# Performance work log

Hardware: AMD Instinct MI355X
Metric: run time of the kernel (lower is better)

Reference implementation:

```python
import jax, jax.numpy as jnp
import numpy as np

VOCAB, H, E, B, S = 50257, 1024, 1024, 64, 2048


def setup_inputs() -> dict:
    key = jax.random.key(0)
    ks = jax.random.split(key, 12)
    s = 0.02
    return {
        "input_seq": jax.random.randint(ks[0], (B,), 0, VOCAB),
        "last_hidden": jax.random.normal(ks[1], (1, B, H), jnp.float32),
        "last_cell": jax.random.normal(ks[2], (1, B, H), jnp.float32),
        "encoder_outputs": jax.random.normal(ks[3], (S, B, H), jnp.float32),
        "emb_W": jax.random.normal(ks[4], (VOCAB, E), jnp.float32) * s,
        "W_ih": jax.random.normal(ks[5], (4 * H, E), jnp.float32) * s,
        "W_hh": jax.random.normal(ks[6], (4 * H, H), jnp.float32) * s,
        "b_ih": jnp.zeros((4 * H,), jnp.float32),
        "b_hh": jnp.zeros((4 * H,), jnp.float32),
        "concat_W": jax.random.normal(ks[7], (H, 2 * H), jnp.float32) * s,
        "concat_b": jnp.zeros((H,), jnp.float32),
        "out_W": jax.random.normal(ks[8], (VOCAB, H), jnp.float32) * s,
        "out_b": jnp.zeros((VOCAB,), jnp.float32),
    }


def reference(input_seq, last_hidden, last_cell, encoder_outputs,
              emb_W, W_ih, W_hh, b_ih, b_hh,
              concat_W, concat_b, out_W, out_b):
    # Embedding lookup (dropout is identity in eval mode)
    x = emb_W[input_seq]                      # [B, E]
    h0 = last_hidden[0]                       # [B, H]
    c0 = last_cell[0]                         # [B, H]
    # Single LSTM step (PyTorch gate order: i, f, g, o)
    gates = x @ W_ih.T + b_ih + h0 @ W_hh.T + b_hh   # [B, 4H]
    i, f, g, o = jnp.split(gates, 4, axis=-1)
    c = jax.nn.sigmoid(f) * c0 + jax.nn.sigmoid(i) * jnp.tanh(g)
    h = jax.nn.sigmoid(o) * jnp.tanh(c)       # [B, H] == rnn_output
    # 'dot' attention: energies[b, s] = h[b] . enc[s, b]  (vectorized)
    energies = jnp.einsum('bh,sbh->bs', h, encoder_outputs)   # [B, S]
    attn = jax.nn.softmax(energies, axis=1)                   # [B, S]
    context = jnp.einsum('bs,sbh->bh', attn, encoder_outputs) # [B, H]
    concat_out = jnp.tanh(jnp.concatenate([h, context], axis=1) @ concat_W.T + concat_b)
    output = concat_out @ out_W.T + out_b                     # [B, VOCAB]
    return output, h[None], c[None], attn[:, None, :]
```

## Files before the change

### kernel.cpp

```cpp
#include <hip/hip_runtime.h>
#include <hip/hip_bf16.h>
#include <math.h>

#define BB 64
#define HH 1024
#define SS 2048
#define VV 50257

typedef float f32x4 __attribute__((ext_vector_type(4)));
typedef short bf16x8 __attribute__((ext_vector_type(8)));

__device__ __forceinline__ float sigf(float x){ return 1.0f/(1.0f+__expf(-x)); }
__device__ __forceinline__ short f2bf(float f){
  __hip_bfloat16 h = __float2bfloat16(f);
  return __builtin_bit_cast(short, h);
}

__global__ __launch_bounds__(256)
void k_gates(const int* __restrict__ seq, const float* __restrict__ embW,
             const float* __restrict__ h0,
             const float* __restrict__ W_ih, const float* __restrict__ W_hh,
             float* __restrict__ dst)
{
  __shared__ float As[64][33];
  __shared__ float Ws[128][33];
  const int tid = threadIdx.x;
  const int nb = blockIdx.x, sk = blockIdx.y, SK = gridDim.y;
  const int tps = 64 / SK;
  const int t0 = sk * tps;
  const int bg = tid & 15, ng = tid >> 4;

  float acc[4][8];
  #pragma unroll
  for (int i = 0; i < 4; ++i)
    #pragma unroll
    for (int j = 0; j < 8; ++j) acc[i][j] = 0.f;

  const int ar = tid >> 2, ac = (tid & 3) * 8;
  const int wr = tid >> 1, wc = (tid & 1) * 16;
  const int wn = nb * 128 + wr;
  const int erow = seq[ar];

  for (int t = t0; t < t0 + tps; ++t) {
    const int kt = t << 5;
    const float* abase; const float* wbase;
    if (kt < 1024) {
      abase = embW + (size_t)erow*1024 + kt;
      wbase = W_ih + (size_t)wn*1024 + kt;
    } else {
      abase = h0 + (size_t)ar*1024 + (kt - 1024);
      wbase = W_hh + (size_t)wn*1024 + (kt - 1024);
    }
    {
      const float* s = abase + ac;
      float4 v0 = *(const float4*)s;
      float4 v1 = *(const float4*)(s + 4);
      As[ar][ac+0]=v0.x; As[ar][ac+1]=v0.y; As[ar][ac+2]=v0.z; As[ar][ac+3]=v0.w;
      As[ar][ac+4]=v1.x; As[ar][ac+5]=v1.y; As[ar][ac+6]=v1.z; As[ar][ac+7]=v1.w;
    }
    {
      const float* s = wbase + wc;
      float4 v0 = *(const float4*)s;
      float4 v1 = *(const float4*)(s + 4);
      float4 v2 = *(const float4*)(s + 8);
      float4 v3 = *(const float4*)(s + 12);
      Ws[wr][wc+0]=v0.x;  Ws[wr][wc+1]=v0.y;  Ws[wr][wc+2]=v0.z;  Ws[wr][wc+3]=v0.w;
      Ws[wr][wc+4]=v1.x;  Ws[wr][wc+5]=v1.y;  Ws[wr][wc+6]=v1.z;  Ws[wr][wc+7]=v1.w;
      Ws[wr][wc+8]=v2.x;  Ws[wr][wc+9]=v2.y;  Ws[wr][wc+10]=v2.z; Ws[wr][wc+11]=v2.w;
      Ws[wr][wc+12]=v3.x; Ws[wr][wc+13]=v3.y; Ws[wr][wc+14]=v3.z; Ws[wr][wc+15]=v3.w;
    }
    __syncthreads();
    #pragma unroll 8
    for (int k = 0; k < 32; ++k) {
      const float a0 = As[bg*4+0][k], a1 = As[bg*4+1][k];
      const float a2 = As[bg*4+2][k], a3 = As[bg*4+3][k];
      #pragma unroll
      for (int j = 0; j < 8; ++j) {
        const float w = Ws[ng*8+j][k];
        acc[0][j] += a0*w; acc[1][j] += a1*w; acc[2][j] += a2*w; acc[3][j] += a3*w;
      }
    }
    __syncthreads();
  }

  #pragma unroll
  for (int j = 0; j < 8; ++j) {
    const int n = nb*128 + ng*8 + j;
    #pragma unroll
    for (int i = 0; i < 4; ++i)
      dst[((size_t)sk*64 + (bg*4+i))*4096 + n] = acc[i][j];
  }
}

__global__ void k_rlstm(const float* __restrict__ part, const float* __restrict__ b_ih,
                        const float* __restrict__ b_hh, const float* __restrict__ c0,
                        float* __restrict__ h_out, float* __restrict__ c_out,
                        short* __restrict__ concA, int SK){
  int idx = blockIdx.x*256 + threadIdx.x;
  int b = idx >> 10, k = idx & 1023;
  float gi = b_ih[k]      + b_hh[k];
  float gf = b_ih[1024+k] + b_hh[1024+k];
  float gg = b_ih[2048+k] + b_hh[2048+k];
  float go = b_ih[3072+k] + b_hh[3072+k];
  const float* p = part + (size_t)b*4096 + k;
  for (int s = 0; s < SK; ++s) {
    const float* ps = p + (size_t)s*64*4096;
    gi += ps[0]; gf += ps[1024]; gg += ps[2048]; go += ps[3072];
  }
  float c = sigf(gf)*c0[idx] + sigf(gi)*tanhf(gg);
  float h = sigf(go)*tanhf(c);
  c_out[idx] = c;
  h_out[idx] = h;
  concA[(size_t)b*2048 + k] = f2bf(h);
}

__global__ __launch_bounds__(256)
void k_mfma(const short* __restrict__ A, int lda,
            const float* __restrict__ W1, int ldw,
            float* __restrict__ dst, int N, int Ktot)
{
  const int tid  = threadIdx.x;
  const int wave = tid >> 6, lane = tid & 63;
  const int nb = blockIdx.x, sk = blockIdx.y, SK = gridDim.y;
  const int ksteps = Ktot >> 5;
  const int kps = ksteps / SK;
  const int k0 = sk * kps;
  const int n0 = nb*128 + wave*32;
  const int r = lane & 15, g = lane >> 4;

  f32x4 acc[4][2] = {};

  for (int ks = k0; ks < k0 + kps; ++ks) {
    const int kk = (ks << 5) + g*8;
    bf16x8 af[4];
    #pragma unroll
    for (int mf = 0; mf < 4; ++mf)
      af[mf] = *(const bf16x8*)(A + (size_t)(mf*16 + r)*lda + kk);
    #pragma unroll
    for (int nf = 0; nf < 2; ++nf) {
      const int n = n0 + nf*16 + r;
      const float* wp = W1 + (size_t)n*ldw + kk;
      float4 w0 = *(const float4*)wp;
      float4 w1 = *(const float4*)(wp + 4);
      bf16x8 bfr;
      bfr[0]=f2bf(w0.x); bfr[1]=f2bf(w0.y); bfr[2]=f2bf(w0.z); bfr[3]=f2bf(w0.w);
      bfr[4]=f2bf(w1.x); bfr[5]=f2bf(w1.y); bfr[6]=f2bf(w1.z); bfr[7]=f2bf(w1.w);
      #pragma unroll
      for (int mf = 0; mf < 4; ++mf)
        acc[mf][nf] = __builtin_amdgcn_mfma_f32_16x16x32_bf16(af[mf], bfr, acc[mf][nf], 0, 0, 0);
    }
  }

  #pragma unroll
  for (int nf = 0; nf < 2; ++nf) {
    const int n = n0 + nf*16 + r;
    #pragma unroll
    for (int mf = 0; mf < 4; ++mf)
      #pragma unroll
      for (int j = 0; j < 4; ++j)
        dst[((size_t)sk*64 + (mf*16 + g*4 + j))*N + n] = acc[mf][nf][j];
  }
}

__global__ void k_reduce(const float* __restrict__ part, const float* __restrict__ bias,
                         short* __restrict__ dstb, int N, int SK){
  size_t idx = (size_t)blockIdx.x*256 + threadIdx.x;
  if (idx >= (size_t)64*N) return;
  int b = (int)(idx / N), n = (int)(idx % N);
  float v = bias[n];
  for (int s = 0; s < SK; ++s) v += part[((size_t)s*64 + b)*N + n];
  dstb[(size_t)b*N + n] = f2bf(tanhf(v));
}

__global__ __launch_bounds__(256)
void k_logits(const short* __restrict__ A, const float* __restrict__ W,
              const float* __restrict__ bias, float* __restrict__ out)
{
  const int tid = threadIdx.x;
  const int wave = tid >> 6, lane = tid & 63;
  const int r = lane & 15, g = lane >> 4;
  const int n0 = blockIdx.x*128 + wave*32;
  const int nA = n0 + r, nB = n0 + 16 + r;
  const float* wA = W + (size_t)(nA < VV ? nA : 0)*1024;
  const float* wB = W + (size_t)(nB < VV ? nB : 0)*1024;
  const short* A0 = A + (size_t)r*1024 + g*8;

  f32x4 acc[4][2] = {};

  bf16x8 a0,a1,a2,a3; float4 u0,u1,v0,v1;
  {
    const int kk = g*8;
    a0 = *(const bf16x8*)(A0);
    a1 = *(const bf16x8*)(A0 + 16*1024);
    a2 = *(const bf16x8*)(A0 + 32*1024);
    a3 = *(const bf16x8*)(A0 + 48*1024);
    u0 = *(const float4*)(wA + kk); u1 = *(const float4*)(wA + kk + 4);
    v0 = *(const float4*)(wB + kk); v1 = *(const float4*)(wB + kk + 4);
  }

  #pragma unroll
  for (int ks = 0; ks < 32; ++ks) {
    bf16x8 ca0=a0, ca1=a1, ca2=a2, ca3=a3;
    float4 cu0=u0, cu1=u1, cv0=v0, cv1=v1;
    if (ks < 31) {
      const int kk = (ks+1)*32 + g*8;
      a0 = *(const bf16x8*)(A0 + (ks+1)*32);
      a1 = *(const bf16x8*)(A0 + 16*1024 + (ks+1)*32);
      a2 = *(const bf16x8*)(A0 + 32*1024 + (ks+1)*32);
      a3 = *(const bf16x8*)(A0 + 48*1024 + (ks+1)*32);
      u0 = *(const float4*)(wA + kk); u1 = *(const float4*)(wA + kk + 4);
      v0 = *(const float4*)(wB + kk); v1 = *(const float4*)(wB + kk + 4);
    }
    bf16x8 bA, bB;
    bA[0]=f2bf(cu0.x); bA[1]=f2bf(cu0.y); bA[2]=f2bf(cu0.z); bA[3]=f2bf(cu0.w);
    bA[4]=f2bf(cu1.x); bA[5]=f2bf(cu1.y); bA[6]=f2bf(cu1.z); bA[7]=f2bf(cu1.w);
    bB[0]=f2bf(cv0.x); bB[1]=f2bf(cv0.y); bB[2]=f2bf(cv0.z); bB[3]=f2bf(cv0.w);
    bB[4]=f2bf(cv1.x); bB[5]=f2bf(cv1.y); bB[6]=f2bf(cv1.z); bB[7]=f2bf(cv1.w);
    acc[0][0] = __builtin_amdgcn_mfma_f32_16x16x32_bf16(ca0, bA, acc[0][0], 0,0,0);
    acc[1][0] = __builtin_amdgcn_mfma_f32_16x16x32_bf16(ca1, bA, acc[1][0], 0,0,0);
    acc[2][0] = __builtin_amdgcn_mfma_f32_16x16x32_bf16(ca2, bA, acc[2][0], 0,0,0);
    acc[3][0] = __builtin_amdgcn_mfma_f32_16x16x32_bf16(ca3, bA, acc[3][0], 0,0,0);
    acc[0][1] = __builtin_amdgcn_mfma_f32_16x16x32_bf16(ca0, bB, acc[0][1], 0,0,0);
    acc[1][1] = __builtin_amdgcn_mfma_f32_16x16x32_bf16(ca1, bB, acc[1][1], 0,0,0);
    acc[2][1] = __builtin_amdgcn_mfma_f32_16x16x32_bf16(ca2, bB, acc[2][1], 0,0,0);
    acc[3][1] = __builtin_amdgcn_mfma_f32_16x16x32_bf16(ca3, bB, acc[3][1], 0,0,0);
  }

  #pragma unroll
  for (int nf = 0; nf < 2; ++nf) {
    const int n = n0 + nf*16 + r;
    if (n < VV) {
      const float bv = bias[n];
      #pragma unroll
      for (int mf = 0; mf < 4; ++mf)
        #pragma unroll
        for (int j = 0; j < 4; ++j)
          out[(size_t)(mf*16 + g*4 + j)*VV + n] = acc[mf][nf][j] + bv;
    }
  }
}

__global__ __launch_bounds__(256)
void k_attn_part(const float* __restrict__ h, const float* __restrict__ enc,
                 float* __restrict__ energ, float* __restrict__ mpart,
                 float* __restrict__ lpart, float* __restrict__ ctxpart, int C){
  const int b  = blockIdx.x & 63;
  const int ch = blockIdx.x >> 6;
  const int wave = threadIdx.x >> 6;
  const int lane = threadIdx.x & 63;
  const int rows = SS / C;
  const int rpw  = rows >> 2;
  const int sw = ch*rows + wave*rpw;

  float4 hv0, hv1, hv2, hv3;
  {
    const float* hb = h + (size_t)b*HH + lane*16;
    hv0 = *(const float4*)(hb);   hv1 = *(const float4*)(hb+4);
    hv2 = *(const float4*)(hb+8); hv3 = *(const float4*)(hb+12);
  }
  float m = -INFINITY, l = 0.f;
  float cacc[16];
  #pragma unroll
  for (int j = 0; j < 16; ++j) cacc[j] = 0.f;

  for (int i = 0; i < rpw; i += 2) {
    const float* ep = enc + ((size_t)(sw+i)*BB + b)*HH + lane*16;
    const float* fp = ep + (size_t)BB*HH;
    const float4 e0 = *(const float4*)(ep);
    const float4 e1 = *(const float4*)(ep+4);
    const float4 e2 = *(const float4*)(ep+8);
    const float4 e3 = *(const float4*)(ep+12);
    const float4 f0 = *(const float4*)(fp);
    const float4 f1 = *(const float4*)(fp+4);
    const float4 f2 = *(const float4*)(fp+8);
    const float4 f3 = *(const float4*)(fp+12);
    float p = hv0.x*e0.x + hv0.y*e0.y + hv0.z*e0.z + hv0.w*e0.w
            + hv1.x*e1.x + hv1.y*e1.y + hv1.z*e1.z + hv1.w*e1.w
            + hv2.x*e2.x + hv2.y*e2.y + hv2.z*e2.z + hv2.w*e2.w
            + hv3.x*e3.x + hv3.y*e3.y + hv3.z*e3.z + hv3.w*e3.w;
    float q = hv0.x*f0.x + hv0.y*f0.y + hv0.z*f0.z + hv0.w*f0.w
            + hv1.x*f1.x + hv1.y*f1.y + hv1.z*f1.z + hv1.w*f1.w
            + hv2.x*f2.x + hv2.y*f2.y + hv2.z*f2.z + hv2.w*f2.w
            + hv3.x*f3.x + hv3.y*f3.y + hv3.z*f3.z + hv3.w*f3.w;
    p += __shfl_xor(p, 1);  q += __shfl_xor(q, 1);
    p += __shfl_xor(p, 2);  q += __shfl_xor(q, 2);
    p += __shfl_xor(p, 4);  q += __shfl_xor(q, 4);
    p += __shfl_xor(p, 8);  q += __shfl_xor(q, 8);
    p += __shfl_xor(p, 16); q += __shfl_xor(q, 16);
    p += __shfl_xor(p, 32); q += __shfl_xor(q, 32);
    if (lane == 0) {
      float2 pq; pq.x = p; pq.y = q;
      *(float2*)(energ + (size_t)b*SS + sw + i) = pq;
    }
    const float mn = fmaxf(fmaxf(m, p), q);
    const float sc = __expf(m - mn);
    const float pe = __expf(p - mn);
    const float qe = __expf(q - mn);
    l = l*sc + pe + qe;
    cacc[0] = cacc[0]*sc + pe*e0.x + qe*f0.x;
    cacc[1] = cacc[1]*sc + pe*e0.y + qe*f0.y;
    cacc[2] = cacc[2]*sc + pe*e0.z + qe*f0.z;
    cacc[3] = cacc[3]*sc + pe*e0.w + qe*f0.w;
    cacc[4] = cacc[4]*sc + pe*e1.x + qe*f1.x;
    cacc[5] = cacc[5]*sc + pe*e1.y + qe*f1.y;
    cacc[6] = cacc[6]*sc + pe*e1.z + qe*f1.z;
    cacc[7] = cacc[7]*sc + pe*e1.w + qe*f1.w;
    cacc[8] = cacc[8]*sc + pe*e2.x + qe*f2.x;
    cacc[9] = cacc[9]*sc + pe*e2.y + qe*f2.y;
    cacc[10] = cacc[10]*sc + pe*e2.z + qe*f2.z;
    cacc[11] = cacc[11]*sc + pe*e2.w + qe*f2.w;
    cacc[12] = cacc[12]*sc + pe*e3.x + qe*f3.x;
    cacc[13] = cacc[13]*sc + pe*e3.y + qe*f3.y;
    cacc[14] = cacc[14]*sc + pe*e3.z + qe*f3.z;
    cacc[15] = cacc[15]*sc + pe*e3.w + qe*f3.w;
    m = mn;
  }

  __shared__ float sm[4], sl[4];
  __shared__ float sctx[4][1024];
  if (lane == 0) { sm[wave] = m; sl[wave] = l; }
  __syncthreads();
  const float mg = fmaxf(fmaxf(sm[0], sm[1]), fmaxf(sm[2], sm[3]));
  const float lg = sl[0]*__expf(sm[0]-mg) + sl[1]*__expf(sm[1]-mg)
                 + sl[2]*__expf(sm[2]-mg) + sl[3]*__expf(sm[3]-mg);
  const float scw = __expf(m - mg);
  #pragma unroll
  for (int j = 0; j < 16; ++j) sctx[wave][lane*16 + j] = cacc[j]*scw;
  __syncthreads();
  const int d = threadIdx.x * 4;
  const float4 a0 = *(const float4*)&sctx[0][d];
  const float4 a1 = *(const float4*)&sctx[1][d];
  const float4 a2 = *(const float4*)&sctx[2][d];
  const float4 a3 = *(const float4*)&sctx[3][d];
  float4 rr;
  rr.x = a0.x+a1.x+a2.x+a3.x; rr.y = a0.y+a1.y+a2.y+a3.y;
  rr.z = a0.z+a1.z+a2.z+a3.z; rr.w = a0.w+a1.w+a2.w+a3.w;
  *(float4*)(ctxpart + ((size_t)(b*C + ch))*HH + d) = rr;
  if (threadIdx.x == 0) { mpart[b*C+ch] = mg; lpart[b*C+ch] = lg; }
}

__global__ void k_attn_fin(const float* __restrict__ mpart, const float* __restrict__ lpart,
                           const float* __restrict__ ctxpart, const float* __restrict__ energ,
                           float* __restrict__ attn, short* __restrict__ concA, int C){
  const int b = blockIdx.x, tid = threadIdx.x;
  float m = -INFINITY;
  for (int c = 0; c < C; ++c) m = fmaxf(m, mpart[b*C+c]);
  float l = 0.f;
  for (int c = 0; c < C; ++c) l += lpart[b*C+c] * __expf(mpart[b*C+c] - m);
  const float inv = 1.0f / l;
  float ax = 0.f, ay = 0.f, az = 0.f, aw = 0.f;
  for (int c = 0; c < C; ++c) {
    const float w = __expf(mpart[b*C+c] - m);
    const float* cp = ctxpart + ((size_t)(b*C+c))*HH + tid*4;
    ax += w*cp[0]; ay += w*cp[1]; az += w*cp[2]; aw += w*cp[3];
  }
  ax *= inv; ay *= inv; az *= inv; aw *= inv;
  short* ca = concA + (size_t)b*2048 + 1024 + tid*4;
  ca[0] = f2bf(ax); ca[1] = f2bf(ay); ca[2] = f2bf(az); ca[3] = f2bf(aw);
  for (int j = 0; j < 8; ++j) {
    const int s = j*256 + tid;
    attn[(size_t)b*SS + s] = __expf(energ[(size_t)b*SS + s] - m) * inv;
  }
}

extern "C" void kernel_launch(void* const* d_in, const int* in_sizes, int n_in,
                              void* d_out, int out_size, void* d_ws, size_t ws_size,
                              hipStream_t stream){
  const int*   seq  = (const int*)  d_in[0];
  const float* h0   = (const float*)d_in[1];
  const float* c0   = (const float*)d_in[2];
  const float* enc  = (const float*)d_in[3];
  const float* embW = (const float*)d_in[4];
  const float* W_ih = (const float*)d_in[5];
  const float* W_hh = (const float*)d_in[6];
  const float* b_ih = (const float*)d_in[7];
  const float* b_hh = (const float*)d_in[8];
  const float* cW   = (const float*)d_in[9];
  const float* cb   = (const float*)d_in[10];
  const float* oW   = (const float*)d_in[11];
  const float* ob   = (const float*)d_in[12];
  float* out = (float*)d_out;

  float* ws = (float*)d_ws;
  const size_t o_energ = 0;
  const size_t o_concA = 131072;
  const size_t o_concB = 196608;
  const size_t o_mp    = 229376;
  const size_t SKPART  = 4194304;
  int C = 32;
  for (;;) {
    size_t need = (o_mp + (size_t)64*C*2 + (size_t)64*C*1024 + SKPART) * sizeof(float);
    if (need <= ws_size || C == 1) break;
    C >>= 1;
  }
  float* energ   = ws + o_energ;
  short* concA   = (short*)(ws + o_concA);
  short* concB   = (short*)(ws + o_concB);
  float* mpart   = ws + o_mp;
  float* lpart   = mpart + (size_t)64*C;
  float* ctxpart = lpart + (size_t)64*C;
  float* skpart  = ctxpart + (size_t)64*C*1024;

  const size_t o_h = 3216448, o_c = 3281984, o_attn = 3347520;

  k_gates<<<dim3(32,16), 256, 0, stream>>>(seq, embW, h0, W_ih, W_hh, skpart);
  k_rlstm<<<256, 256, 0, stream>>>(skpart, b_ih, b_hh, c0, out + o_h, out + o_c,
                                   concA, 16);
  k_attn_part<<<64*C, 256, 0, stream>>>(out + o_h, enc, energ, mpart, lpart, ctxpart, C);
  k_attn_fin<<<64, 256, 0, stream>>>(mpart, lpart, ctxpart, energ, out + o_attn, concA, C);
  k_mfma<<<dim3(8,16), 256, 0, stream>>>(concA, 2048, cW, 2048, skpart, 1024, 2048);
  k_reduce<<<256, 256, 0, stream>>>(skpart, cb, concB, 1024, 16);
  k_logits<<<393, 256, 0, stream>>>(concB, oW, ob, out);
}
```

Before: 267.4 us.

## Use split-bf16 MFMA for LSTM gates and split-K the logits GEMM

Replaces the fp32 LDS-tiled gates GEMM with an MFMA kernel that splits activations and weights into hi/lo bf16 parts (three MFMAs per tile) to keep near-fp32 accuracy, fed by a new prep kernel that converts the gathered embedding and hidden state. Separately, the logits kernel now splits K across two wave pairs per block, doubling the grid to 786 blocks, and reduces the halves through shared memory. It also double-buffers the loads with even/odd register sets. The aim is better occupancy and bandwidth use on the large out_W stream, at the cost of an extra launch and an LDS reduction.

```diff
diff --git a/kernel.cpp b/kernel.cpp
--- a/kernel.cpp
+++ b/kernel.cpp
@@ -15,80 +15,89 @@
   __hip_bfloat16 h = __float2bfloat16(f);
   return __builtin_bit_cast(short, h);
 }
-
-__global__ __launch_bounds__(256)
-void k_gates(const int* __restrict__ seq, const float* __restrict__ embW,
-             const float* __restrict__ h0,
+__device__ __forceinline__ float bf2f(short s){
+  __hip_bfloat16 h = __builtin_bit_cast(__hip_bfloat16, s);
+  return __bfloat162float(h);
+}
+
+__global__ void k_prep(const int* __restrict__ seq, const float* __restrict__ embW,
+                       const float* __restrict__ h0,
+                       short* __restrict__ Ahi, short* __restrict__ Alo){
+  const int b = blockIdx.x;
+  const int k = threadIdx.x * 8;
+  const float* src = (k < 1024) ? (embW + (size_t)seq[b]*1024 + k)
+                                : (h0 + (size_t)b*1024 + (k - 1024));
+  float4 v0 = *(const float4*)src;
+  float4 v1 = *(const float4*)(src + 4);
+  float v[8] = {v0.x,v0.y,v0.z,v0.w,v1.x,v1.y,v1.z,v1.w};
+  bf16x8 hi, lo;
+  #pragma unroll
+  for (int j = 0; j < 8; ++j) {
+    short h = f2bf(v[j]);
+    hi[j] = h;
+    lo[j] = f2bf(v[j] - bf2f(h));
+  }
+  *(bf16x8*)(Ahi + (size_t)b*2048 + k) = hi;
+  *(bf16x8*)(Alo + (size_t)b*2048 + k) = lo;
+}
+
+__global__ __launch_bounds__(256, 3)
+void k_gates(const short* __restrict__ Ahi, const short* __restrict__ Alo,
              const float* __restrict__ W_ih, const float* __restrict__ W_hh,
              float* __restrict__ dst)
 {
-  __shared__ float As[64][33];
-  __shared__ float Ws[128][33];
   const int tid = threadIdx.x;
-  const int nb = blockIdx.x, sk = blockIdx.y, SK = gridDim.y;
-  const int tps = 64 / SK;
-  const int t0 = sk * tps;
-  const int bg = tid & 15, ng = tid >> 4;
-
-  float acc[4][8];
-  #pragma unroll
-  for (int i = 0; i < 4; ++i)
-    #pragma unroll
-    for (int j = 0; j < 8; ++j) acc[i][j] = 0.f;
-
-  const int ar = tid >> 2, ac = (tid & 3) * 8;
-  const int wr = tid >> 1, wc = (tid & 1) * 16;
-  const int wn = nb * 128 + wr;
-  const int erow = seq[ar];
-
-  for (int t = t0; t < t0 + tps; ++t) {
-    const int kt = t << 5;
-    const float* abase; const float* wbase;
-    if (kt < 1024) {
-      abase = embW + (size_t)erow*1024 + kt;
-      wbase = W_ih + (size_t)wn*1024 + kt;
-    } else {
-      abase = h0 + (size_t)ar*1024 + (kt - 1024);
-      wbase = W_hh + (size_t)wn*1024 + (kt - 1024);
-    }
-    {
-      const float* s = abase + ac;
-      float4 v0 = *(const float4*)s;
-      float4 v1 = *(const float4*)(s + 4);
-      As[ar][ac+0]=v0.x; As[ar][ac+1]=v0.y; As[ar][ac+2]=v0.z; As[ar][ac+3]=v0.w;
-      As[ar][ac+4]=v1.x; As[ar][ac+5]=v1.y; As[ar][ac+6]=v1.z; As[ar][ac+7]=v1.w;
-    }
-    {
-      const float* s = wbase + wc;
-      float4 v0 = *(const float4*)s;
-      float4 v1 = *(const float4*)(s + 4);
-      float4 v2 = *(const float4*)(s + 8);
-      float4 v3 = *(const float4*)(s + 12);
-      Ws[wr][wc+0]=v0.x;  Ws[wr][wc+1]=v0.y;  Ws[wr][wc+2]=v0.z;  Ws[wr][wc+3]=v0.w;
-      Ws[wr][wc+4]=v1.x;  Ws[wr][wc+5]=v1.y;  Ws[wr][wc+6]=v1.z;  Ws[wr][wc+7]=v1.w;
-      Ws[wr][wc+8]=v2.x;  Ws[wr][wc+9]=v2.y;  Ws[wr][wc+10]=v2.z; Ws[wr][wc+11]=v2.w;
-      Ws[wr][wc+12]=v3.x; Ws[wr][wc+13]=v3.y; Ws[wr][wc+14]=v3.z; Ws[wr][wc+15]=v3.w;
-    }
-    __syncthreads();
-    #pragma unroll 8
-    for (int k = 0; k < 32; ++k) {
-      const float a0 = As[bg*4+0][k], a1 = As[bg*4+1][k];
-      const float a2 = As[bg*4+2][k], a3 = As[bg*4+3][k];
+  const int wave = tid >> 6, lane = tid & 63;
+  const int r = lane & 15, g = lane >> 4;
+  const int nb = blockIdx.x, sk = blockIdx.y;
+  const int n0 = nb*128 + wave*32;
+  const int kbase = sk*128;
+  const float* Wm = (kbase < 1024) ? W_ih : W_hh;
+  const int kw = (kbase < 1024) ? kbase : (kbase - 1024);
+
+  f32x4 acc[4][2] = {};
+
+  #pragma unroll
+  for (int ks = 0; ks < 4; ++ks) {
+    const int kk = kbase + ks*32 + g*8;
+    const int ko = kw   + ks*32 + g*8;
+    bf16x8 ahi[4], alo[4];
+    #pragma unroll
+    for (int mf = 0; mf < 4; ++mf) {
+      ahi[mf] = *(const bf16x8*)(Ahi + (size_t)(mf*16 + r)*2048 + kk);
+      alo[mf] = *(const bf16x8*)(Alo + (size_t)(mf*16 + r)*2048 + kk);
+    }
+    #pragma unroll
+    for (int nf = 0; nf < 2; ++nf) {
+      const int n = n0 + nf*16 + r;
+      const float* wp = Wm + (size_t)n*1024 + ko;
+      float4 w0 = *(const float4*)wp;
+      float4 w1 = *(const float4*)(wp + 4);
+      float wv[8] = {w0.x,w0.y,w0.z,w0.w,w1.x,w1.y,w1.z,w1.w};
+      bf16x8 whi, wlo;
       #pragma unroll
       for (int j = 0; j < 8; ++j) {
-        const float w = Ws[ng*8+j][k];
-        acc[0][j] += a0*w; acc[1][j] += a1*w; acc[2][j] += a2*w; acc[3][j] += a3*w;
+        short h = f2bf(wv[j]);
+        whi[j] = h;
+        wlo[j] = f2bf(wv[j] - bf2f(h));
       }
-    }
-    __syncthreads();
-  }
-
-  #pragma unroll
-  for (int j = 0; j < 8; ++j) {
-    const int n = nb*128 + ng*8 + j;
-    #pragma unroll
-    for (int i = 0; i < 4; ++i)
-      dst[((size_t)sk*64 + (bg*4+i))*4096 + n] = acc[i][j];
+      #pragma unroll
+      for (int mf = 0; mf < 4; ++mf) {
+        acc[mf][nf] = __builtin_amdgcn_mfma_f32_16x16x32_bf16(ahi[mf], whi, acc[mf][nf], 0,0,0);
+        acc[mf][nf] = __builtin_amdgcn_mfma_f32_16x16x32_bf16(alo[mf], whi, acc[mf][nf], 0,0,0);
+        acc[mf][nf] = __builtin_amdgcn_mfma_f32_16x16x32_bf16(ahi[mf], wlo, acc[mf][nf], 0,0,0);
+      }
+    }
+  }
+
+  #pragma unroll
+  for (int nf = 0; nf < 2; ++nf) {
+    const int n = n0 + nf*16 + r;
+    #pragma unroll
+    for (int mf = 0; mf < 4; ++mf)
+      #pragma unroll
+      for (int j = 0; j < 4; ++j)
+        dst[((size_t)sk*64 + (mf*16 + g*4 + j))*4096 + n] = acc[mf][nf][j];
   }
 }
 
@@ -172,70 +181,104 @@
   dstb[(size_t)b*N + n] = f2bf(tanhf(v));
 }
 
-__global__ __launch_bounds__(256)
+__global__ __launch_bounds__(256, 3)
 void k_logits(const short* __restrict__ A, const float* __restrict__ W,
               const float* __restrict__ bias, float* __restrict__ out)
 {
   const int tid = threadIdx.x;
   const int wave = tid >> 6, lane = tid & 63;
   const int r = lane & 15, g = lane >> 4;
-  const int n0 = blockIdx.x*128 + wave*32;
+  const int cg = wave & 1, kh = wave >> 1;
+  const int n0 = blockIdx.x*64 + cg*32;
   const int nA = n0 + r, nB = n0 + 16 + r;
-  const float* wA = W + (size_t)(nA < VV ? nA : 0)*1024;
-  const float* wB = W + (size_t)(nB < VV ? nB : 0)*1024;
-  const short* A0 = A + (size_t)r*1024 + g*8;
+  const int nAc = (nA < VV) ? nA : 0;
+  const int nBc = (nB < VV) ? nB : 0;
+  const int kb = kh * 512;
+
+  const short* A0 = A + (size_t)r*1024       + kb + g*8;
+  const short* A1 = A + (size_t)(16+r)*1024  + kb + g*8;
+  const short* A2 = A + (size_t)(32+r)*1024  + kb + g*8;
+  const short* A3 = A + (size_t)(48+r)*1024  + kb + g*8;
+  const float* wA = W + (size_t)nAc*1024 + kb + g*8;
+  const float* wB = W + (size_t)nBc*1024 + kb + g*8;
 
   f32x4 acc[4][2] = {};
 
-  bf16x8 a0,a1,a2,a3; float4 u0,u1,v0,v1;
-  {
-    const int kk = g*8;
-    a0 = *(const bf16x8*)(A0);
-    a1 = *(const bf16x8*)(A0 + 16*1024);
-    a2 = *(const bf16x8*)(A0 + 32*1024);
-    a3 = *(const bf16x8*)(A0 + 48*1024);
-    u0 = *(const float4*)(wA + kk); u1 = *(const float4*)(wA + kk + 4);
-    v0 = *(const float4*)(wB + kk); v1 = *(const float4*)(wB + kk + 4);
-  }
-
-  #pragma unroll
-  for (int ks = 0; ks < 32; ++ks) {
-    bf16x8 ca0=a0, ca1=a1, ca2=a2, ca3=a3;
-    float4 cu0=u0, cu1=u1, cv0=v0, cv1=v1;
-    if (ks < 31) {
-      const int kk = (ks+1)*32 + g*8;
-      a0 = *(const bf16x8*)(A0 + (ks+1)*32);
-      a1 = *(const bf16x8*)(A0 + 16*1024 + (ks+1)*32);
-      a2 = *(const bf16x8*)(A0 + 32*1024 + (ks+1)*32);
-      a3 = *(const bf16x8*)(A0 + 48*1024 + (ks+1)*32);
-      u0 = *(const float4*)(wA + kk); u1 = *(const float4*)(wA + kk + 4);
-      v0 = *(const float4*)(wB + kk); v1 = *(const float4*)(wB + kk + 4);
-    }
-    bf16x8 bA, bB;
-    bA[0]=f2bf(cu0.x); bA[1]=f2bf(cu0.y); bA[2]=f2bf(cu0.z); bA[3]=f2bf(cu0.w);
-    bA[4]=f2bf(cu1.x); bA[5]=f2bf(cu1.y); bA[6]=f2bf(cu1.z); bA[7]=f2bf(cu1.w);
-    bB[0]=f2bf(cv0.x); bB[1]=f2bf(cv0.y); bB[2]=f2bf(cv0.z); bB[3]=f2bf(cv0.w);
-    bB[4]=f2bf(cv1.x); bB[5]=f2bf(cv1.y); bB[6]=f2bf(cv1.z); bB[7]=f2bf(cv1.w);
-    acc[0][0] = __builtin_amdgcn_mfma_f32_16x16x32_bf16(ca0, bA, acc[0][0], 0,0,0);
-    acc[1][0] = __builtin_amdgcn_mfma_f32_16x16x32_bf16(ca1, bA, acc[1][0], 0,0,0);
-    acc[2][0] = __builtin_amdgcn_mfma_f32_16x16x32_bf16(ca2, bA, acc[2][0], 0,0,0);
-    acc[3][0] = __builtin_amdgcn_mfma_f32_16x16x32_bf16(ca3, bA, acc[3][0], 0,0,0);
-    acc[0][1] = __builtin_amdgcn_mfma_f32_16x16x32_bf16(ca0, bB, acc[0][1], 0,0,0);
-    acc[1][1] = __builtin_amdgcn_mfma_f32_16x16x32_bf16(ca1, bB, acc[1][1], 0,0,0);
-    acc[2][1] = __builtin_amdgcn_mfma_f32_16x16x32_bf16(ca2, bB, acc[2][1], 0,0,0);
-    acc[3][1] = __builtin_amdgcn_mfma_f32_16x16x32_bf16(ca3, bB, acc[3][1], 0,0,0);
-  }
-
-  #pragma unroll
-  for (int nf = 0; nf < 2; ++nf) {
-    const int n = n0 + nf*16 + r;
-    if (n < VV) {
-      const float bv = bias[n];
+  bf16x8 aE0,aE1,aE2,aE3, aO0,aO1,aO2,aO3;
+  float4 wEA0,wEA1,wEB0,wEB1, wOA0,wOA1,wOB0,wOB1;
+
+#define LOAD_E(KS) { const int o=(KS)*32; \
+    aE0=*(const bf16x8*)(A0+o); aE1=*(const bf16x8*)(A1+o); \
+    aE2=*(const bf16x8*)(A2+o); aE3=*(const bf16x8*)(A3+o); \
+    wEA0=*(const float4*)(wA+o); wEA1=*(const float4*)(wA+o+4); \
+    wEB0=*(const float4*)(wB+o); wEB1=*(const float4*)(wB+o+4); }
+#define LOAD_O(KS) { const int o=(KS)*32; \
+    aO0=*(const bf16x8*)(A0+o); aO1=*(const bf16x8*)(A1+o); \
+    aO2=*(const bf16x8*)(A2+o); aO3=*(const bf16x8*)(A3+o); \
+    wOA0=*(const float4*)(wA+o); wOA1=*(const float4*)(wA+o+4); \
+    wOB0=*(const float4*)(wB+o); wOB1=*(const float4*)(wB+o+4); }
+#define CVT(bdst, w0, w1) { \
+    bdst[0]=f2bf(w0.x); bdst[1]=f2bf(w0.y); bdst[2]=f2bf(w0.z); bdst[3]=f2bf(w0.w); \
+    bdst[4]=f2bf(w1.x); bdst[5]=f2bf(w1.y); bdst[6]=f2bf(w1.z); bdst[7]=f2bf(w1.w); }
+#define MM(a0_,a1_,a2_,a3_,bA_,bB_) { \
+    acc[0][0]=__builtin_amdgcn_mfma_f32_16x16x32_bf16(a0_,bA_,acc[0][0],0,0,0); \
+    acc[1][0]=__builtin_amdgcn_mfma_f32_16x16x32_bf16(a1_,bA_,acc[1][0],0,0,0); \
+    acc[2][0]=__builtin_amdgcn_mfma_f32_16x16x32_bf16(a2_,bA_,acc[2][0],0,0,0); \
+    acc[3][0]=__builtin_amdgcn_mfma_f32_16x16x32_bf16(a3_,bA_,acc[3][0],0,0,0); \
+    acc[0][1]=__builtin_amdgcn_mfma_f32_16x16x32_bf16(a0_,bB_,acc[0][1],0,0,0); \
+    acc[1][1]=__builtin_amdgcn_mfma_f32_16x16x32_bf16(a1_,bB_,acc[1][1],0,0,0); \
+    acc[2][1]=__builtin_amdgcn_mfma_f32_16x16x32_bf16(a2_,bB_,acc[2][1],0,0,0); \
+    acc[3][1]=__builtin_amdgcn_mfma_f32_16x16x32_bf16(a3_,bB_,acc[3][1],0,0,0); }
+
+  LOAD_E(0);
+  LOAD_O(1);
+  #pragma unroll
+  for (int it = 0; it < 8; ++it) {
+    const int ks = it*2;
+    {
+      bf16x8 bA, bB;
+      CVT(bA, wEA0, wEA1); CVT(bB, wEB0, wEB1);
+      bf16x8 ca0=aE0, ca1=aE1, ca2=aE2, ca3=aE3;
+      if (it < 7) LOAD_E(ks+2);
+      MM(ca0,ca1,ca2,ca3,bA,bB);
+    }
+    {
+      bf16x8 bA, bB;
+      CVT(bA, wOA0, wOA1); CVT(bB, wOB0, wOB1);
+      bf16x8 ca0=aO0, ca1=aO1, ca2=aO2, ca3=aO3;
+      if (it < 7) LOAD_O(ks+3);
+      MM(ca0,ca1,ca2,ca3,bA,bB);
+    }
+  }
+#undef LOAD_E
+#undef LOAD_O
+#undef CVT
+#undef MM
+
+  __shared__ float red[2][32][64];
+  if (kh) {
+    #pragma unroll
+    for (int nf = 0; nf < 2; ++nf)
       #pragma unroll
       for (int mf = 0; mf < 4; ++mf)
         #pragma unroll
         for (int j = 0; j < 4; ++j)
-          out[(size_t)(mf*16 + g*4 + j)*VV + n] = acc[mf][nf][j] + bv;
+          red[cg][nf*16 + mf*4 + j][lane] = acc[mf][nf][j];
+  }
+  __syncthreads();
+  if (!kh) {
+    #pragma unroll
+    for (int nf = 0; nf < 2; ++nf) {
+      const int n = n0 + nf*16 + r;
+      if (n < VV) {
+        const float bv = bias[n];
+        #pragma unroll
+        for (int mf = 0; mf < 4; ++mf)
+          #pragma unroll
+          for (int j = 0; j < 4; ++j)
+            out[(size_t)(mf*16 + g*4 + j)*VV + n] =
+                acc[mf][nf][j] + red[cg][nf*16 + mf*4 + j][lane] + bv;
+      }
     }
   }
 }
@@ -385,7 +428,9 @@
   const size_t o_energ = 0;
   const size_t o_concA = 131072;
   const size_t o_concB = 196608;
-  const size_t o_mp    = 229376;
+  const size_t o_Ahi   = 229376;
+  const size_t o_Alo   = 294912;
+  const size_t o_mp    = 360448;
   const size_t SKPART  = 4194304;
   int C = 32;
   for (;;) {
@@ -396,6 +441,8 @@
   float* energ   = ws + o_energ;
   short* concA   = (short*)(ws + o_concA);
   short* concB   = (short*)(ws + o_concB);
+  short* Ahi     = (short*)(ws + o_Ahi);
+  short* Alo     = (short*)(ws + o_Alo);
   float* mpart   = ws + o_mp;
   float* lpart   = mpart + (size_t)64*C;
   float* ctxpart = lpart + (size_t)64*C;
@@ -403,12 +450,13 @@
 
   const size_t o_h = 3216448, o_c = 3281984, o_attn = 3347520;
 
-  k_gates<<<dim3(32,16), 256, 0, stream>>>(seq, embW, h0, W_ih, W_hh, skpart);
+  k_prep<<<64, 256, 0, stream>>>(seq, embW, h0, Ahi, Alo);
+  k_gates<<<dim3(32,16), 256, 0, stream>>>(Ahi, Alo, W_ih, W_hh, skpart);
   k_rlstm<<<256, 256, 0, stream>>>(skpart, b_ih, b_hh, c0, out + o_h, out + o_c,
                                    concA, 16);
   k_attn_part<<<64*C, 256, 0, stream>>>(out + o_h, enc, energ, mpart, lpart, ctxpart, C);
   k_attn_fin<<<64, 256, 0, stream>>>(mpart, lpart, ctxpart, energ, out + o_attn, concA, C);
   k_mfma<<<dim3(8,16), 256, 0, stream>>>(concA, 2048, cW, 2048, skpart, 1024, 2048);
   k_reduce<<<256, 256, 0, stream>>>(skpart, cb, concB, 1024, 16);
-  k_logits<<<393, 256, 0, stream>>>(concB, oW, ob, out);
-}
+  k_logits<<<786, 256, 0, stream>>>(concB, oW, ob, out);
+}
```

After: 258.8 us. 1.03x faster.
